# Performance work log

Measured on AMD Instinct MI355X. Metric: run time of the kernel, lower is better.

The kernel has to match this reference:

```python
import jax, jax.numpy as jnp
import numpy as np

N_NODES = 20000
N_EDGES = 50000
IN_DIM = 128
HID = 128
OUT_DIM = 64
N_PAIRS = 128
N_LAYERS = 2
N_HEADS = 4


def setup_inputs() -> dict:
    key = jax.random.key(0)
    ks = jax.random.split(key, 32)
    s = 0.05
    def p(k, shape):
        return jax.random.normal(k, shape, jnp.float32) * s
    inp = {}
    inp["node_features"] = jax.random.normal(ks[0], (N_NODES, IN_DIM), jnp.float32)
    inp["edge_index"] = jax.random.randint(ks[1], (2, N_EDGES), 0, N_NODES, jnp.int32)
    inp["edge_timestamps"] = jax.random.uniform(ks[2], (N_EDGES,), jnp.float32)
    inp["target_pairs"] = jax.random.randint(ks[3], (N_PAIRS, 2), 0, N_NODES, jnp.int32)
    inp["in_W"] = p(ks[4], (HID, IN_DIM)); inp["in_b"] = p(ks[5], (HID,))
    inp["te_W1"] = p(ks[6], (N_LAYERS, HID, 1)); inp["te_b1"] = p(ks[7], (N_LAYERS, HID))
    inp["te_W2"] = p(ks[8], (N_LAYERS, HID, HID)); inp["te_b2"] = p(ks[9], (N_LAYERS, HID))
    inp["attn_in_W"] = p(ks[10], (N_LAYERS, 3 * HID, HID)); inp["attn_in_b"] = p(ks[11], (N_LAYERS, 3 * HID))
    inp["attn_out_W"] = p(ks[12], (N_LAYERS, HID, HID)); inp["attn_out_b"] = p(ks[13], (N_LAYERS, HID))
    inp["ft_W"] = p(ks[14], (N_LAYERS, HID, HID)); inp["ft_b"] = p(ks[15], (N_LAYERS, HID))
    inp["op_W"] = p(ks[16], (N_LAYERS, HID, HID)); inp["op_b"] = p(ks[17], (N_LAYERS, HID))
    inp["out1_W"] = p(ks[18], (HID, HID)); inp["out1_b"] = p(ks[19], (HID,))
    inp["out2_W"] = p(ks[20], (OUT_DIM, HID)); inp["out2_b"] = p(ks[21], (OUT_DIM,))
    inp["lp1_W"] = p(ks[22], (HID, 2 * OUT_DIM)); inp["lp1_b"] = p(ks[23], (HID,))
    inp["lp2_W"] = p(ks[24], (HID // 2, HID)); inp["lp2_b"] = p(ks[25], (HID // 2,))
    inp["lp3_W"] = p(ks[26], (1, HID // 2)); inp["lp3_b"] = p(ks[27], (1,))
    return inp


def _forward(node_features, edge_index, edge_timestamps, target_pairs,
             in_W, in_b, te_W1, te_b1, te_W2, te_b2,
             attn_in_W, attn_in_b, attn_out_W, attn_out_b,
             ft_W, ft_b, op_W, op_b,
             out1_W, out1_b, out2_W, out2_b,
             lp1_W, lp1_b, lp2_W, lp2_b, lp3_W, lp3_b):
    N = node_features.shape[0]
    h = in_W.shape[0]
    H = N_HEADS
    d = h // H
    scale = 1.0 / np.sqrt(d).astype(np.float32)
    src, dst = edge_index[0], edge_index[1]
    # flattened target nodes; duplicates compute identical rows so dedup (torch.unique) is unneeded
    targets = target_pairs.reshape(-1)  # [U]
    U = targets.shape[0]
    E = src.shape[0]

    x = node_features @ in_W.T + in_b  # [N, h]
    for l in range(te_W1.shape[0]):
        tf = x @ ft_W[l].T + ft_b[l]                                           # [N, h]
        tfeat = jax.nn.relu(edge_timestamps[:, None] @ te_W1[l].T + te_b1[l])
        tfeat = tfeat @ te_W2[l].T + te_b2[l]                                  # [E, h]
        Wq, Wk, Wv = jnp.split(attn_in_W[l], 3, axis=0)
        bq, bk, bv = jnp.split(attn_in_b[l], 3)
        q = (tf[targets] @ Wq.T + bq).reshape(U, H, d)
        # keys/values are linear in (tf[nbr] + tfeat): split into node term A and edge term B
        Ak = (tf @ Wk.T).reshape(N, H, d)
        Bk = (tfeat @ Wk.T + bk).reshape(E, H, d)
        Av = (tf @ Wv.T).reshape(N, H, d)
        Bv = (tfeat @ Wv.T + bv).reshape(E, H, d)
        is_src = src[None, :] == targets[:, None]          # [U, E]
        mask = is_src | (dst[None, :] == targets[:, None])  # edge incident to target
        nbr = jnp.where(is_src, dst[None, :], src[None, :])  # other endpoint, [U, E]
        qAk = jnp.einsum('uhd,nhd->uhn', q, Ak) * scale      # [U, H, N]
        idx = jnp.broadcast_to(nbr[:, None, :], (U, H, E))
        s_node = jnp.take_along_axis(qAk, idx, axis=2)        # [U, H, E]
        s_edge = jnp.einsum('uhd,ehd->uhe', q, Bk) * scale
        scores = jnp.where(mask[:, None, :], s_node + s_edge, -1e30)
        p = jax.nn.softmax(scores, axis=-1)
        p = jnp.where(mask[:, None, :], p, 0.0)               # [U, H, E]
        out_edge = jnp.einsum('uhe,ehd->uhd', p, Bv)
        # sum_e p * Av[nbr] via per-target scatter of probs into node space
        w = jax.vmap(lambda pe, ne: jax.ops.segment_sum(pe, ne, num_segments=N))(
            p.transpose(0, 2, 1), nbr)                        # [U, N, H]
        out_node = jnp.einsum('unh,nhd->uhd', w, Av)
        attn = (out_node + out_edge).reshape(U, h) @ attn_out_W[l].T + attn_out_b[l]
        has_nbr = mask.any(axis=1)
        agg_in = jnp.where(has_nbr[:, None], attn, tf[targets])
        agg = agg_in @ op_W[l].T + op_b[l]
        x = x.at[targets].set(agg)
        x = jax.nn.relu(x)
    emb = jax.nn.relu(x @ out1_W.T + out1_b) @ out2_W.T + out2_b  # [N, out]
    pair = jnp.concatenate([emb[target_pairs[:, 0]], emb[target_pairs[:, 1]]], axis=1)
    z = jax.nn.relu(pair @ lp1_W.T + lp1_b)
    z = jax.nn.relu(z @ lp2_W.T + lp2_b)
    return jax.nn.sigmoid(z @ lp3_W.T + lp3_b)  # [B, 1]


def reference(node_features, edge_index, edge_timestamps, target_pairs,
              in_W, in_b, te_W1, te_b1, te_W2, te_b2,
              attn_in_W, attn_in_b, attn_out_W, attn_out_b,
              ft_W, ft_b, op_W, op_b,
              out1_W, out1_b, out2_W, out2_b,
              lp1_W, lp1_b, lp2_W, lp2_b, lp3_W, lp3_b):
    return _forward(node_features, edge_index, edge_timestamps, target_pairs,
                    in_W, in_b, te_W1, te_b1, te_W2, te_b2,
                    attn_in_W, attn_in_b, attn_out_W, attn_out_b,
                    ft_W, ft_b, op_W, op_b,
                    out1_W, out1_b, out2_W, out2_b,
                    lp1_W, lp1_b, lp2_W, lp2_b, lp3_W, lp3_b)
```

## Files before the change

### kernel.cpp

```cpp
#include <hip/hip_runtime.h>
#include <math.h>

#define N_NODES 20000
#define N_EDGES 50000
#define N_SLOTS 256
#define N_PAIRS 128
#define CAP 64
#define MSTRIDE 16384
#define NMAT 19

__device__ __forceinline__ float4 relu4(float4 v) {
    return make_float4(fmaxf(v.x, 0.f), fmaxf(v.y, 0.f), fmaxf(v.z, 0.f), fmaxf(v.w, 0.f));
}
__device__ __forceinline__ float4 add4(float4 a, float4 b) {
    return make_float4(a.x + b.x, a.y + b.y, a.z + b.z, a.w + b.w);
}
__device__ __forceinline__ void fma4(float4& acc, const float4 w, const float s) {
    acc.x = fmaf(w.x, s, acc.x); acc.y = fmaf(w.y, s, acc.y);
    acc.z = fmaf(w.z, s, acc.z); acc.w = fmaf(w.w, s, acc.w);
}
#define F4Z make_float4(0.f, 0.f, 0.f, 0.f)

__device__ __forceinline__ float4 mv_ks1(const float* __restrict__ WT,
                                         const float* __restrict__ xv128,
                                         int g, int jj) {
    const float4* W4 = (const float4*)WT;
    const float4* x4 = (const float4*)xv128;
    float4 acc = F4Z;
#pragma unroll 2
    for (int kk4 = 0; kk4 < 8; ++kk4) {
        int k4 = g * 8 + kk4;
        float4 xv = x4[k4];
        fma4(acc, W4[(k4 * 4 + 0) * 32 + jj], xv.x);
        fma4(acc, W4[(k4 * 4 + 1) * 32 + jj], xv.y);
        fma4(acc, W4[(k4 * 4 + 2) * 32 + jj], xv.z);
        fma4(acc, W4[(k4 * 4 + 3) * 32 + jj], xv.w);
    }
    return acc;
}
__device__ __forceinline__ float4 mv_ks1_64(const float* __restrict__ WT,
                                            const float* __restrict__ xv128,
                                            int g, int jj) {
    const float4* W4 = (const float4*)WT;
    const float4* x4 = (const float4*)xv128;
    int j16 = jj & 15;
    float4 acc = F4Z;
#pragma unroll 2
    for (int kk4 = 0; kk4 < 8; ++kk4) {
        int k4 = g * 8 + kk4;
        float4 xv = x4[k4];
        fma4(acc, W4[(k4 * 4 + 0) * 16 + j16], xv.x);
        fma4(acc, W4[(k4 * 4 + 1) * 16 + j16], xv.y);
        fma4(acc, W4[(k4 * 4 + 2) * 16 + j16], xv.z);
        fma4(acc, W4[(k4 * 4 + 3) * 16 + j16], xv.w);
    }
    return acc;
}
__device__ __forceinline__ float4 comb1(const float4* pb, int jj) {
    return add4(add4(pb[jj], pb[32 + jj]), add4(pb[64 + jj], pb[96 + jj]));
}

__device__ __forceinline__ float4 mv_ks1_g8(const float* __restrict__ WT,
                                            const float* __restrict__ xv128,
                                            int g, int jj) {
    const float4* W4 = (const float4*)WT;
    const float4* x4 = (const float4*)xv128;
    float4 acc = F4Z;
#pragma unroll
    for (int kk4 = 0; kk4 < 4; ++kk4) {
        int k4 = g * 4 + kk4;
        float4 xv = x4[k4];
        fma4(acc, W4[(k4 * 4 + 0) * 32 + jj], xv.x);
        fma4(acc, W4[(k4 * 4 + 1) * 32 + jj], xv.y);
        fma4(acc, W4[(k4 * 4 + 2) * 32 + jj], xv.z);
        fma4(acc, W4[(k4 * 4 + 3) * 32 + jj], xv.w);
    }
    return acc;
}
__device__ __forceinline__ void mv8_g8(const float* __restrict__ WT,
                                       const float* __restrict__ xs,
                                       int g, int jj, float4* acc) {
    const float4* W4 = (const float4*)WT;
    const float4* x4 = (const float4*)xs;
#pragma unroll
    for (int kk4 = 0; kk4 < 4; ++kk4) {
        int k4 = g * 4 + kk4;
        float4 w0 = W4[(k4 * 4 + 0) * 32 + jj];
        float4 w1 = W4[(k4 * 4 + 1) * 32 + jj];
        float4 w2 = W4[(k4 * 4 + 2) * 32 + jj];
        float4 w3 = W4[(k4 * 4 + 3) * 32 + jj];
#pragma unroll
        for (int e = 0; e < 8; ++e) {
            float4 xv = x4[e * 32 + k4];
            fma4(acc[e], w0, xv.x); fma4(acc[e], w1, xv.y);
            fma4(acc[e], w2, xv.z); fma4(acc[e], w3, xv.w);
        }
    }
}
__device__ __forceinline__ float4 comb1_g8(const float4* pb, int jj) {
    float4 s = pb[jj];
#pragma unroll
    for (int gp = 1; gp < 8; ++gp) s = add4(s, pb[gp * 32 + jj]);
    return s;
}
__device__ __forceinline__ float4 comb8_g8(const float4* pb, int it, int jj) {
    float4 s = pb[it * 32 + jj];
#pragma unroll
    for (int gp = 1; gp < 8; ++gp) s = add4(s, pb[(gp * 8 + it) * 32 + jj]);
    return s;
}


__global__ __launch_bounds__(256) void k_prep_tr(
    const int* __restrict__ ei, const int* __restrict__ tp,
    const float* __restrict__ inW, const float* __restrict__ ftW,
    const float* __restrict__ teW2, const float* __restrict__ aiW,
    const float* __restrict__ aoW, const float* __restrict__ opW,
    const float* __restrict__ o1W, const float* __restrict__ o2W,
    const float* __restrict__ l1W, const float* __restrict__ l2W,
    float* __restrict__ WT, int* __restrict__ cnt, int2* __restrict__ lst) {
    __shared__ float tile[32][129];
    __shared__ int lc;
    const int b = blockIdx.x;
    if (threadIdx.x == 0) lc = 0;
    if (b < 72) {
        int m, r0, rows;
        if (b < 68) { m = b >> 2; r0 = (b & 3) * 32; rows = 128; }
        else { int mm = b - 68; m = 17 + (mm >> 1); r0 = (mm & 1) * 32; rows = 64; }
        const float* src;
        if (m == 0) src = inW;
        else if (m <= 2) src = ftW + (m - 1) * MSTRIDE;
        else if (m <= 4) src = teW2 + (m - 3) * MSTRIDE;
        else if (m <= 10) src = aiW + (m - 5) * MSTRIDE;
        else if (m <= 12) src = aoW + (m - 11) * MSTRIDE;
        else if (m <= 14) src = opW + (m - 13) * MSTRIDE;
        else if (m == 15) src = o1W;
        else if (m == 16) src = l1W;
        else if (m == 17) src = o2W;
        else src = l2W;
        float* dst = WT + m * MSTRIDE;
        for (int idx = threadIdx.x; idx < 32 * 128; idx += 256) {
            int r = idx >> 7, c = idx & 127;
            tile[r][c] = src[(r0 + r) * 128 + c];
        }
        __syncthreads();
        for (int idx = threadIdx.x; idx < 128 * 32; idx += 256) {
            int k = idx >> 5, jr = idx & 31;
            dst[k * rows + r0 + jr] = tile[jr][k];
        }
    }
    __syncthreads();
    const int u = tp[b];
    const int4* src4 = (const int4*)ei;
    const int4* dst4 = (const int4*)(ei + N_EDGES);
    for (int e4 = threadIdx.x; e4 < N_EDGES / 4; e4 += 256) {
        int4 s = src4[e4];
        int4 d = dst4[e4];
        int ss[4] = {s.x, s.y, s.z, s.w};
        int dd[4] = {d.x, d.y, d.z, d.w};
#pragma unroll
        for (int t = 0; t < 4; ++t) {
            if (ss[t] == u || dd[t] == u) {
                int nbr = (ss[t] == u) ? dd[t] : ss[t];
                int pos = atomicAdd(&lc, 1);
                if (pos < CAP) lst[b * CAP + pos] = make_int2(e4 * 4 + t, nbr);
            }
        }
    }
    __syncthreads();
    if (threadIdx.x == 0) cnt[b] = lc;
}

__global__ __launch_bounds__(256) void k_edge(
    const float* __restrict__ nf, const float* __restrict__ x,
    const float* __restrict__ ts, const int* __restrict__ tp,
    const int* __restrict__ cnt, const int2* __restrict__ lst,
    const float* __restrict__ WT_in, const float* __restrict__ inb,
    const float* __restrict__ WT_ft, const float* __restrict__ ftb,
    const float* __restrict__ teW1, const float* __restrict__ teb1,
    const float* __restrict__ WT_te2, const float* __restrict__ teb2,
    const float* __restrict__ WT_q, const float* __restrict__ bq,
    const float* __restrict__ WT_k, const float* __restrict__ bk,
    const float* __restrict__ WT_v, const float* __restrict__ bv,
    float* __restrict__ x_out, float* __restrict__ tfu_g,
    float* __restrict__ scores, float* __restrict__ vbuf, int layer) {
    __shared__ __align__(16) float xu[128], x0u[128], tfv[128], qv[128];
    __shared__ __align__(16) float xs[8 * 128], t1s[8 * 128], x0s[8 * 128], zs[8 * 128];
    __shared__ __align__(16) float4 pb[8 * 8 * 32];
    __shared__ int nbr_s[8];
    __shared__ float ts_s[8];
    const int slot = blockIdx.x, tid = threadIdx.x, g = tid >> 5, jj = tid & 31;
    const float scale = 0.17677669529663687f;
    const int u = tp[slot];
    const int c = min(cnt[slot], CAP);

    if (tid < 128) xu[tid] = (layer == 0) ? nf[(size_t)u * 128 + tid]
                                          : x[(size_t)u * 128 + tid];
    __syncthreads();
    const float* xeff = xu;
    if (layer == 0) {
        pb[g * 32 + jj] = mv_ks1_g8(WT_in, xu, g, jj);
        __syncthreads();
        if (g == 0)
            *(float4*)(x0u + jj * 4) = add4(comb1_g8(pb, jj), *(const float4*)(inb + jj * 4));
        xeff = x0u;
        __syncthreads();
    }
    pb[g * 32 + jj] = mv_ks1_g8(WT_ft, xeff, g, jj);
    __syncthreads();
    if (g == 0) {
        float4 t = add4(comb1_g8(pb, jj), *(const float4*)(ftb + jj * 4));
        *(float4*)(tfv + jj * 4) = t;
        *(float4*)(tfu_g + (size_t)slot * 128 + jj * 4) = t;
    }
    __syncthreads();
    pb[g * 32 + jj] = mv_ks1_g8(WT_q, tfv, g, jj);
    __syncthreads();
    if (g == 0)
        *(float4*)(qv + jj * 4) = add4(comb1_g8(pb, jj), *(const float4*)(bq + jj * 4));
    __syncthreads();

    for (int base = 0; base < c; base += 8) {
        if (tid < 8) {
            int i = base + tid;
            int2 en = (i < c) ? lst[slot * CAP + i] : make_int2(0, 0);
            nbr_s[tid] = en.y;
            ts_s[tid] = (i < c) ? ts[en.x] : 0.f;
        }
        __syncthreads();
        {
            int e = tid >> 5, c0 = jj * 4;
            const float* srcp = (layer == 0) ? (nf + (size_t)nbr_s[e] * 128 + c0)
                                             : (x + (size_t)nbr_s[e] * 128 + c0);
            float4 v = *(const float4*)srcp;
            float* dstp = (layer == 0) ? xs : x0s;
            *(float4*)(dstp + e * 128 + c0) = v;
            float tse = ts_s[e];
            float4 w = *(const float4*)(teW1 + c0);
            float4 b = *(const float4*)(teb1 + c0);
            *(float4*)(t1s + e * 128 + c0) =
                make_float4(fmaxf(fmaf(tse, w.x, b.x), 0.f),
                            fmaxf(fmaf(tse, w.y, b.y), 0.f),
                            fmaxf(fmaf(tse, w.z, b.z), 0.f),
                            fmaxf(fmaf(tse, w.w, b.w), 0.f));
        }
        __syncthreads();
        if (layer == 0) {
            float4 acc[8] = {F4Z, F4Z, F4Z, F4Z, F4Z, F4Z, F4Z, F4Z};
            mv8_g8(WT_in, xs, g, jj, acc);
#pragma unroll
            for (int e = 0; e < 8; ++e) pb[(g * 8 + e) * 32 + jj] = acc[e];
            __syncthreads();
            {
                float4 x0v = add4(comb8_g8(pb, g, jj), *(const float4*)(inb + jj * 4));
                *(float4*)(x0s + g * 128 + jj * 4) = x0v;
                if (base + g < c)
                    *(float4*)(x_out + (size_t)nbr_s[g] * 128 + jj * 4) = relu4(x0v);
            }
            __syncthreads();
        }
        float4 za, zb;
        {
            float4 acc[8] = {F4Z, F4Z, F4Z, F4Z, F4Z, F4Z, F4Z, F4Z};
            mv8_g8(WT_ft, x0s, g, jj, acc);
#pragma unroll
            for (int e = 0; e < 8; ++e) pb[(g * 8 + e) * 32 + jj] = acc[e];
            __syncthreads();
            za = comb8_g8(pb, g, jj);
            __syncthreads();
            float4 acc2[8] = {F4Z, F4Z, F4Z, F4Z, F4Z, F4Z, F4Z, F4Z};
            mv8_g8(WT_te2, t1s, g, jj, acc2);
#pragma unroll
            for (int e = 0; e < 8; ++e) pb[(g * 8 + e) * 32 + jj] = acc2[e];
            __syncthreads();
            zb = comb8_g8(pb, g, jj);
            float4 z4 = add4(add4(za, zb),
                             add4(*(const float4*)(ftb + jj * 4),
                                  *(const float4*)(teb2 + jj * 4)));
            *(float4*)(zs + g * 128 + jj * 4) = z4;
            __syncthreads();
        }
        {
            float4 acc[8] = {F4Z, F4Z, F4Z, F4Z, F4Z, F4Z, F4Z, F4Z};
            mv8_g8(WT_k, zs, g, jj, acc);
#pragma unroll
            for (int e = 0; e < 8; ++e) pb[(g * 8 + e) * 32 + jj] = acc[e];
            __syncthreads();
            float4 kk = add4(comb8_g8(pb, g, jj), *(const float4*)(bk + jj * 4));
            __syncthreads();
            float4 acc2[8] = {F4Z, F4Z, F4Z, F4Z, F4Z, F4Z, F4Z, F4Z};
            mv8_g8(WT_v, zs, g, jj, acc2);
#pragma unroll
            for (int e = 0; e < 8; ++e) pb[(g * 8 + e) * 32 + jj] = acc2[e];
            __syncthreads();
            float4 vv = add4(comb8_g8(pb, g, jj), *(const float4*)(bv + jj * 4));
            float4 q4 = *(const float4*)(qv + jj * 4);
            float pr = q4.x * kk.x + q4.y * kk.y + q4.z * kk.z + q4.w * kk.w;
            pr += __shfl_xor(pr, 1);
            pr += __shfl_xor(pr, 2);
            pr += __shfl_xor(pr, 4);
            if (base + g < c) {
                int pos = slot * CAP + base + g;
                if ((jj & 7) == 0) scores[pos * 4 + (jj >> 3)] = pr * scale;
                *(float4*)(vbuf + (size_t)pos * 128 + jj * 4) = vv;
            }
            __syncthreads();
        }
    }
}

__global__ __launch_bounds__(128) void k_reduce(
    const int* __restrict__ cnt, const int* __restrict__ tp,
    const float* __restrict__ scores, const float* __restrict__ vbuf,
    const float* __restrict__ tfu_g,
    const float* __restrict__ WT_ao, const float* __restrict__ aob,
    const float* __restrict__ WT_op, const float* __restrict__ opb,
    float* __restrict__ x,
    const float* __restrict__ WT_o1, const float* __restrict__ o1b,
    const float* __restrict__ WT_o2, const float* __restrict__ o2b,
    float* __restrict__ emb, int mode) {
    __shared__ __align__(16) float outv[128], zv[128], xt[128], e1[128];
    __shared__ __align__(16) float4 pb[4 * 32];
    const int slot = blockIdx.x, tid = threadIdx.x, g = tid >> 5, jj = tid & 31;
    const int j = tid, h = j >> 5;
    const int u = tp[slot];
    const int c = min(cnt[slot], CAP);
    if (c > 0) {
        float m = -INFINITY;
        for (int i = 0; i < c; ++i) m = fmaxf(m, scores[(slot * CAP + i) * 4 + h]);
        float l = 0.f, o = 0.f;
        for (int i = 0; i < c; ++i) {
            float p = __expf(scores[(slot * CAP + i) * 4 + h] - m);
            l += p;
            o = fmaf(p, vbuf[(size_t)(slot * CAP + i) * 128 + j], o);
        }
        outv[j] = o / l;
    } else {
        outv[j] = 0.f;
    }
    __syncthreads();
    pb[g * 32 + jj] = mv_ks1(WT_ao, outv, g, jj);
    __syncthreads();
    if (g == 0) {
        float4 z4;
        if (c > 0) z4 = add4(comb1(pb, jj), *(const float4*)(aob + jj * 4));
        else z4 = *(const float4*)(tfu_g + (size_t)slot * 128 + jj * 4);
        *(float4*)(zv + jj * 4) = z4;
    }
    __syncthreads();
    pb[g * 32 + jj] = mv_ks1(WT_op, zv, g, jj);
    __syncthreads();
    if (mode == 0) {
        if (g == 0) {
            float4 a = relu4(add4(comb1(pb, jj), *(const float4*)(opb + jj * 4)));
            *(float4*)(x + (size_t)u * 128 + jj * 4) = a;
        }
        return;
    }
    if (g == 0)
        *(float4*)(xt + jj * 4) = relu4(add4(comb1(pb, jj), *(const float4*)(opb + jj * 4)));
    __syncthreads();
    pb[g * 32 + jj] = mv_ks1(WT_o1, xt, g, jj);
    __syncthreads();
    if (g == 0)
        *(float4*)(e1 + jj * 4) = relu4(add4(comb1(pb, jj), *(const float4*)(o1b + jj * 4)));
    __syncthreads();
    pb[g * 32 + jj] = mv_ks1_64(WT_o2, e1, g, jj);
    __syncthreads();
    if (g == 0 && jj < 16)
        *(float4*)(emb + (size_t)slot * 64 + jj * 4) =
            add4(comb1(pb, jj), *(const float4*)(o2b + jj * 4));
}

__global__ __launch_bounds__(128) void k_pair(
    const float* __restrict__ emb,
    const float* __restrict__ WT_l1, const float* __restrict__ l1b,
    const float* __restrict__ WT_l2, const float* __restrict__ l2b,
    const float* __restrict__ l3W, const float* __restrict__ l3b,
    float* __restrict__ out) {
    __shared__ __align__(16) float pv[128], z1[128], z2s[64];
    __shared__ __align__(16) float4 pb[4 * 32];
    const int p = blockIdx.x, tid = threadIdx.x, g = tid >> 5, jj = tid & 31;
    pv[tid] = (tid < 64) ? emb[(size_t)(2 * p) * 64 + tid]
                         : emb[(size_t)(2 * p + 1) * 64 + (tid - 64)];
    __syncthreads();
    pb[g * 32 + jj] = mv_ks1(WT_l1, pv, g, jj);
    __syncthreads();
    if (g == 0)
        *(float4*)(z1 + jj * 4) = relu4(add4(comb1(pb, jj), *(const float4*)(l1b + jj * 4)));
    __syncthreads();
    pb[g * 32 + jj] = mv_ks1_64(WT_l2, z1, g, jj);
    __syncthreads();
    if (g == 0 && jj < 16)
        *(float4*)(z2s + jj * 4) = relu4(add4(comb1(pb, jj), *(const float4*)(l2b + jj * 4)));
    __syncthreads();
    if (tid < 64) {
        float v = z2s[tid] * l3W[tid];
        v += __shfl_xor(v, 1);
        v += __shfl_xor(v, 2);
        v += __shfl_xor(v, 4);
        v += __shfl_xor(v, 8);
        v += __shfl_xor(v, 16);
        v += __shfl_xor(v, 32);
        if (tid == 0) out[p] = 1.f / (1.f + __expf(-(v + l3b[0])));
    }
}

extern "C" void kernel_launch(void* const* d_in, const int* in_sizes, int n_in,
                              void* d_out, int out_size, void* d_ws, size_t ws_size,
                              hipStream_t stream) {
    const float* nf  = (const float*)d_in[0];
    const int*   ei  = (const int*)d_in[1];
    const float* ts  = (const float*)d_in[2];
    const int*   tp  = (const int*)d_in[3];
    const float* inW = (const float*)d_in[4];
    const float* inb = (const float*)d_in[5];
    const float* teW1 = (const float*)d_in[6];
    const float* teb1 = (const float*)d_in[7];
    const float* teW2 = (const float*)d_in[8];
    const float* teb2 = (const float*)d_in[9];
    const float* aiW = (const float*)d_in[10];
    const float* aib = (const float*)d_in[11];
    const float* aoW = (const float*)d_in[12];
    const float* aob = (const float*)d_in[13];
    const float* ftW = (const float*)d_in[14];
    const float* ftb = (const float*)d_in[15];
    const float* opW = (const float*)d_in[16];
    const float* opb = (const float*)d_in[17];
    const float* o1W = (const float*)d_in[18];
    const float* o1b = (const float*)d_in[19];
    const float* o2W = (const float*)d_in[20];
    const float* o2b = (const float*)d_in[21];
    const float* l1W = (const float*)d_in[22];
    const float* l1b = (const float*)d_in[23];
    const float* l2W = (const float*)d_in[24];
    const float* l2b = (const float*)d_in[25];
    const float* l3W = (const float*)d_in[26];
    const float* l3b = (const float*)d_in[27];
    float* out = (float*)d_out;

    char* ws = (char*)d_ws;
    size_t off = 0;
    float* x    = (float*)(ws + off); off += (size_t)N_NODES * 128 * 4;
    int*   cnt  = (int*)  (ws + off); off += N_SLOTS * 4;
    int2*  lst  = (int2*) (ws + off); off += (size_t)N_SLOTS * CAP * 8;
    float* tfu  = (float*)(ws + off); off += N_SLOTS * 128 * 4;
    float* emb  = (float*)(ws + off); off += N_SLOTS * 64 * 4;
    float* scb  = (float*)(ws + off); off += (size_t)N_SLOTS * CAP * 4 * 4;
    float* vbuf = (float*)(ws + off); off += (size_t)N_SLOTS * CAP * 128 * 4;
    float* WT   = (float*)(ws + off); off += (size_t)NMAT * MSTRIDE * 4;

    k_prep_tr<<<N_SLOTS, 256, 0, stream>>>(ei, tp, inW, ftW, teW2, aiW, aoW, opW,
                                           o1W, o2W, l1W, l2W, WT, cnt, lst);

    for (int l = 0; l < 2; ++l) {
        const float* WT_ft = WT + (1 + l) * MSTRIDE;
        const float* WT_te2 = WT + (3 + l) * MSTRIDE;
        const float* WT_q = WT + (5 + 3 * l) * MSTRIDE;
        const float* WT_k = WT + (6 + 3 * l) * MSTRIDE;
        const float* WT_v = WT + (7 + 3 * l) * MSTRIDE;
        const float* WT_ao = WT + (11 + l) * MSTRIDE;
        const float* WT_op = WT + (13 + l) * MSTRIDE;
        const float* bq = aib + l * 384;
        k_edge<<<N_SLOTS, 256, 0, stream>>>(
            nf, x, ts, tp, cnt, lst,
            WT, inb, WT_ft, ftb + l * 128, teW1 + l * 128, teb1 + l * 128,
            WT_te2, teb2 + l * 128, WT_q, bq, WT_k, bq + 128, WT_v, bq + 256,
            x, tfu, scb, vbuf, l);
        k_reduce<<<N_SLOTS, 128, 0, stream>>>(
            cnt, tp, scb, vbuf, tfu, WT_ao, aob + l * 128,
            WT_op, opb + l * 128, x,
            WT + 15 * MSTRIDE, o1b, WT + 17 * MSTRIDE, o2b, emb, l);
    }
    k_pair<<<N_PAIRS, 128, 0, stream>>>(emb, WT + 16 * MSTRIDE, l1b,
                                        WT + 18 * MSTRIDE, l2b, l3W, l3b, out);
}
```

Before: 205.1 us.

## Fuse edge and reduce kernels per layer, keep scores and values in shared memory

The per-layer edge kernel and the softmax/reduce kernel are merged into one k_layer kernel. Attention scores and value vectors now stay in shared memory instead of round-tripping through global buffers, and the tf vector is kept on-chip. To avoid a race where a neighbour write in one block would clobber a target row written by another block in the same kernel, the prep kernel marks neighbours that are themselves targets with a flag bit, and those writes are skipped. This removes a launch and global traffic per layer, but raises shared memory per block (about 32KB for the value buffer), which may lower occupancy.

```diff
diff --git a/kernel.cpp b/kernel.cpp
--- a/kernel.cpp
+++ b/kernel.cpp
@@ -8,6 +8,7 @@
 #define CAP 64
 #define MSTRIDE 16384
 #define NMAT 19
+#define TFLAG (1 << 30)
 
 __device__ __forceinline__ float4 relu4(float4 v) {
     return make_float4(fmaxf(v.x, 0.f), fmaxf(v.y, 0.f), fmaxf(v.z, 0.f), fmaxf(v.w, 0.f));
@@ -20,6 +21,74 @@
     acc.z = fmaf(w.z, s, acc.z); acc.w = fmaf(w.w, s, acc.w);
 }
 #define F4Z make_float4(0.f, 0.f, 0.f, 0.f)
+
+__device__ __forceinline__ float4 mv_ks1_g8(const float* __restrict__ WT,
+                                            const float* __restrict__ xv128,
+                                            int g, int jj) {
+    const float4* W4 = (const float4*)WT;
+    const float4* x4 = (const float4*)xv128;
+    float4 acc = F4Z;
+#pragma unroll
+    for (int kk4 = 0; kk4 < 4; ++kk4) {
+        int k4 = g * 4 + kk4;
+        float4 xv = x4[k4];
+        fma4(acc, W4[(k4 * 4 + 0) * 32 + jj], xv.x);
+        fma4(acc, W4[(k4 * 4 + 1) * 32 + jj], xv.y);
+        fma4(acc, W4[(k4 * 4 + 2) * 32 + jj], xv.z);
+        fma4(acc, W4[(k4 * 4 + 3) * 32 + jj], xv.w);
+    }
+    return acc;
+}
+__device__ __forceinline__ float4 mv_ks1_g8_64(const float* __restrict__ WT,
+                                               const float* __restrict__ xv128,
+                                               int g, int jj) {
+    const float4* W4 = (const float4*)WT;
+    const float4* x4 = (const float4*)xv128;
+    int j16 = jj & 15;
+    float4 acc = F4Z;
+#pragma unroll
+    for (int kk4 = 0; kk4 < 4; ++kk4) {
+        int k4 = g * 4 + kk4;
+        float4 xv = x4[k4];
+        fma4(acc, W4[(k4 * 4 + 0) * 16 + j16], xv.x);
+        fma4(acc, W4[(k4 * 4 + 1) * 16 + j16], xv.y);
+        fma4(acc, W4[(k4 * 4 + 2) * 16 + j16], xv.z);
+        fma4(acc, W4[(k4 * 4 + 3) * 16 + j16], xv.w);
+    }
+    return acc;
+}
+__device__ __forceinline__ void mv8_g8(const float* __restrict__ WT,
+                                       const float* __restrict__ xs,
+                                       int g, int jj, float4* acc) {
+    const float4* W4 = (const float4*)WT;
+    const float4* x4 = (const float4*)xs;
+#pragma unroll
+    for (int kk4 = 0; kk4 < 4; ++kk4) {
+        int k4 = g * 4 + kk4;
+        float4 w0 = W4[(k4 * 4 + 0) * 32 + jj];
+        float4 w1 = W4[(k4 * 4 + 1) * 32 + jj];
+        float4 w2 = W4[(k4 * 4 + 2) * 32 + jj];
+        float4 w3 = W4[(k4 * 4 + 3) * 32 + jj];
+#pragma unroll
+        for (int e = 0; e < 8; ++e) {
+            float4 xv = x4[e * 32 + k4];
+            fma4(acc[e], w0, xv.x); fma4(acc[e], w1, xv.y);
+            fma4(acc[e], w2, xv.z); fma4(acc[e], w3, xv.w);
+        }
+    }
+}
+__device__ __forceinline__ float4 comb1_g8(const float4* pb, int jj) {
+    float4 s = pb[jj];
+#pragma unroll
+    for (int gp = 1; gp < 8; ++gp) s = add4(s, pb[gp * 32 + jj]);
+    return s;
+}
+__device__ __forceinline__ float4 comb8_g8(const float4* pb, int it, int jj) {
+    float4 s = pb[it * 32 + jj];
+#pragma unroll
+    for (int gp = 1; gp < 8; ++gp) s = add4(s, pb[(gp * 8 + it) * 32 + jj]);
+    return s;
+}
 
 __device__ __forceinline__ float4 mv_ks1(const float* __restrict__ WT,
                                          const float* __restrict__ xv128,
@@ -60,56 +129,6 @@
     return add4(add4(pb[jj], pb[32 + jj]), add4(pb[64 + jj], pb[96 + jj]));
 }
 
-__device__ __forceinline__ float4 mv_ks1_g8(const float* __restrict__ WT,
-                                            const float* __restrict__ xv128,
-                                            int g, int jj) {
-    const float4* W4 = (const float4*)WT;
-    const float4* x4 = (const float4*)xv128;
-    float4 acc = F4Z;
-#pragma unroll
-    for (int kk4 = 0; kk4 < 4; ++kk4) {
-        int k4 = g * 4 + kk4;
-        float4 xv = x4[k4];
-        fma4(acc, W4[(k4 * 4 + 0) * 32 + jj], xv.x);
-        fma4(acc, W4[(k4 * 4 + 1) * 32 + jj], xv.y);
-        fma4(acc, W4[(k4 * 4 + 2) * 32 + jj], xv.z);
-        fma4(acc, W4[(k4 * 4 + 3) * 32 + jj], xv.w);
-    }
-    return acc;
-}
-__device__ __forceinline__ void mv8_g8(const float* __restrict__ WT,
-                                       const float* __restrict__ xs,
-                                       int g, int jj, float4* acc) {
-    const float4* W4 = (const float4*)WT;
-    const float4* x4 = (const float4*)xs;
-#pragma unroll
-    for (int kk4 = 0; kk4 < 4; ++kk4) {
-        int k4 = g * 4 + kk4;
-        float4 w0 = W4[(k4 * 4 + 0) * 32 + jj];
-        float4 w1 = W4[(k4 * 4 + 1) * 32 + jj];
-        float4 w2 = W4[(k4 * 4 + 2) * 32 + jj];
-        float4 w3 = W4[(k4 * 4 + 3) * 32 + jj];
-#pragma unroll
-        for (int e = 0; e < 8; ++e) {
-            float4 xv = x4[e * 32 + k4];
-            fma4(acc[e], w0, xv.x); fma4(acc[e], w1, xv.y);
-            fma4(acc[e], w2, xv.z); fma4(acc[e], w3, xv.w);
-        }
-    }
-}
-__device__ __forceinline__ float4 comb1_g8(const float4* pb, int jj) {
-    float4 s = pb[jj];
-#pragma unroll
-    for (int gp = 1; gp < 8; ++gp) s = add4(s, pb[gp * 32 + jj]);
-    return s;
-}
-__device__ __forceinline__ float4 comb8_g8(const float4* pb, int it, int jj) {
-    float4 s = pb[it * 32 + jj];
-#pragma unroll
-    for (int gp = 1; gp < 8; ++gp) s = add4(s, pb[(gp * 8 + it) * 32 + jj]);
-    return s;
-}
-
 
 __global__ __launch_bounds__(256) void k_prep_tr(
     const int* __restrict__ ei, const int* __restrict__ tp,
@@ -120,6 +139,7 @@
     const float* __restrict__ l1W, const float* __restrict__ l2W,
     float* __restrict__ WT, int* __restrict__ cnt, int2* __restrict__ lst) {
     __shared__ float tile[32][129];
+    __shared__ int tps[N_SLOTS];
     __shared__ int lc;
     const int b = blockIdx.x;
     if (threadIdx.x == 0) lc = 0;
@@ -149,8 +169,9 @@
             dst[k * rows + r0 + jr] = tile[jr][k];
         }
     }
-    __syncthreads();
-    const int u = tp[b];
+    for (int i = threadIdx.x; i < N_SLOTS; i += 256) tps[i] = tp[i];
+    __syncthreads();
+    const int u = tps[b];
     const int4* src4 = (const int4*)ei;
     const int4* dst4 = (const int4*)(ei + N_EDGES);
     for (int e4 = threadIdx.x; e4 < N_EDGES / 4; e4 += 256) {
@@ -169,9 +190,16 @@
     }
     __syncthreads();
     if (threadIdx.x == 0) cnt[b] = lc;
-}
-
-__global__ __launch_bounds__(256) void k_edge(
+    int c = min(lc, CAP);
+    if (threadIdx.x < c) {
+        int2 en = lst[b * CAP + threadIdx.x];
+        bool ist = false;
+        for (int t = 0; t < N_SLOTS; ++t) ist |= (tps[t] == en.y);
+        if (ist) { en.y |= TFLAG; lst[b * CAP + threadIdx.x] = en; }
+    }
+}
+
+__global__ __launch_bounds__(256) void k_layer(
     const float* __restrict__ nf, const float* __restrict__ x,
     const float* __restrict__ ts, const int* __restrict__ tp,
     const int* __restrict__ cnt, const int2* __restrict__ lst,
@@ -182,12 +210,17 @@
     const float* __restrict__ WT_q, const float* __restrict__ bq,
     const float* __restrict__ WT_k, const float* __restrict__ bk,
     const float* __restrict__ WT_v, const float* __restrict__ bv,
-    float* __restrict__ x_out, float* __restrict__ tfu_g,
-    float* __restrict__ scores, float* __restrict__ vbuf, int layer) {
-    __shared__ __align__(16) float xu[128], x0u[128], tfv[128], qv[128];
+    const float* __restrict__ WT_ao, const float* __restrict__ aob,
+    const float* __restrict__ WT_op, const float* __restrict__ opb,
+    const float* __restrict__ WT_o1, const float* __restrict__ o1b,
+    const float* __restrict__ WT_o2, const float* __restrict__ o2b,
+    float* __restrict__ x_out, float* __restrict__ emb, int layer) {
+    __shared__ __align__(16) float xu[128], x0u[128], tfv[128], qv[128], sv[128];
     __shared__ __align__(16) float xs[8 * 128], t1s[8 * 128], x0s[8 * 128], zs[8 * 128];
     __shared__ __align__(16) float4 pb[8 * 8 * 32];
-    __shared__ int nbr_s[8];
+    __shared__ __align__(16) float vbl[CAP * 128];
+    __shared__ float scl[CAP * 4];
+    __shared__ int nbr_s[8], tf_s[8];
     __shared__ float ts_s[8];
     const int slot = blockIdx.x, tid = threadIdx.x, g = tid >> 5, jj = tid & 31;
     const float scale = 0.17677669529663687f;
@@ -208,11 +241,8 @@
     }
     pb[g * 32 + jj] = mv_ks1_g8(WT_ft, xeff, g, jj);
     __syncthreads();
-    if (g == 0) {
-        float4 t = add4(comb1_g8(pb, jj), *(const float4*)(ftb + jj * 4));
-        *(float4*)(tfv + jj * 4) = t;
-        *(float4*)(tfu_g + (size_t)slot * 128 + jj * 4) = t;
-    }
+    if (g == 0)
+        *(float4*)(tfv + jj * 4) = add4(comb1_g8(pb, jj), *(const float4*)(ftb + jj * 4));
     __syncthreads();
     pb[g * 32 + jj] = mv_ks1_g8(WT_q, tfv, g, jj);
     __syncthreads();
@@ -224,7 +254,8 @@
         if (tid < 8) {
             int i = base + tid;
             int2 en = (i < c) ? lst[slot * CAP + i] : make_int2(0, 0);
-            nbr_s[tid] = en.y;
+            nbr_s[tid] = en.y & ~TFLAG;
+            tf_s[tid] = (en.y & TFLAG) ? 1 : 0;
             ts_s[tid] = (i < c) ? ts[en.x] : 0.f;
         }
         __syncthreads();
@@ -254,26 +285,25 @@
             {
                 float4 x0v = add4(comb8_g8(pb, g, jj), *(const float4*)(inb + jj * 4));
                 *(float4*)(x0s + g * 128 + jj * 4) = x0v;
-                if (base + g < c)
+                if (base + g < c && !tf_s[g])
                     *(float4*)(x_out + (size_t)nbr_s[g] * 128 + jj * 4) = relu4(x0v);
             }
             __syncthreads();
         }
-        float4 za, zb;
         {
             float4 acc[8] = {F4Z, F4Z, F4Z, F4Z, F4Z, F4Z, F4Z, F4Z};
             mv8_g8(WT_ft, x0s, g, jj, acc);
 #pragma unroll
             for (int e = 0; e < 8; ++e) pb[(g * 8 + e) * 32 + jj] = acc[e];
             __syncthreads();
-            za = comb8_g8(pb, g, jj);
+            float4 za = comb8_g8(pb, g, jj);
             __syncthreads();
             float4 acc2[8] = {F4Z, F4Z, F4Z, F4Z, F4Z, F4Z, F4Z, F4Z};
             mv8_g8(WT_te2, t1s, g, jj, acc2);
 #pragma unroll
             for (int e = 0; e < 8; ++e) pb[(g * 8 + e) * 32 + jj] = acc2[e];
             __syncthreads();
-            zb = comb8_g8(pb, g, jj);
+            float4 zb = comb8_g8(pb, g, jj);
             float4 z4 = add4(add4(za, zb),
                              add4(*(const float4*)(ftb + jj * 4),
                                   *(const float4*)(teb2 + jj * 4)));
@@ -300,76 +330,63 @@
             pr += __shfl_xor(pr, 2);
             pr += __shfl_xor(pr, 4);
             if (base + g < c) {
-                int pos = slot * CAP + base + g;
-                if ((jj & 7) == 0) scores[pos * 4 + (jj >> 3)] = pr * scale;
-                *(float4*)(vbuf + (size_t)pos * 128 + jj * 4) = vv;
+                if ((jj & 7) == 0) scl[(base + g) * 4 + (jj >> 3)] = pr * scale;
+                *(float4*)(vbl + (base + g) * 128 + jj * 4) = vv;
             }
             __syncthreads();
         }
     }
-}
-
-__global__ __launch_bounds__(128) void k_reduce(
-    const int* __restrict__ cnt, const int* __restrict__ tp,
-    const float* __restrict__ scores, const float* __restrict__ vbuf,
-    const float* __restrict__ tfu_g,
-    const float* __restrict__ WT_ao, const float* __restrict__ aob,
-    const float* __restrict__ WT_op, const float* __restrict__ opb,
-    float* __restrict__ x,
-    const float* __restrict__ WT_o1, const float* __restrict__ o1b,
-    const float* __restrict__ WT_o2, const float* __restrict__ o2b,
-    float* __restrict__ emb, int mode) {
-    __shared__ __align__(16) float outv[128], zv[128], xt[128], e1[128];
-    __shared__ __align__(16) float4 pb[4 * 32];
-    const int slot = blockIdx.x, tid = threadIdx.x, g = tid >> 5, jj = tid & 31;
-    const int j = tid, h = j >> 5;
-    const int u = tp[slot];
-    const int c = min(cnt[slot], CAP);
-    if (c > 0) {
-        float m = -INFINITY;
-        for (int i = 0; i < c; ++i) m = fmaxf(m, scores[(slot * CAP + i) * 4 + h]);
-        float l = 0.f, o = 0.f;
-        for (int i = 0; i < c; ++i) {
-            float p = __expf(scores[(slot * CAP + i) * 4 + h] - m);
-            l += p;
-            o = fmaf(p, vbuf[(size_t)(slot * CAP + i) * 128 + j], o);
-        }
-        outv[j] = o / l;
-    } else {
-        outv[j] = 0.f;
-    }
-    __syncthreads();
-    pb[g * 32 + jj] = mv_ks1(WT_ao, outv, g, jj);
+
+    if (tid < 128) {
+        int h = tid >> 5;
+        if (c > 0) {
+            float m = -INFINITY;
+            for (int i = 0; i < c; ++i) m = fmaxf(m, scl[i * 4 + h]);
+            float l = 0.f, o = 0.f;
+            for (int i = 0; i < c; ++i) {
+                float p = __expf(scl[i * 4 + h] - m);
+                l += p;
+                o = fmaf(p, vbl[i * 128 + tid], o);
+            }
+            sv[tid] = o / l;
+        } else {
+            sv[tid] = 0.f;
+        }
+    }
+    __syncthreads();
+    pb[g * 32 + jj] = mv_ks1_g8(WT_ao, sv, g, jj);
     __syncthreads();
     if (g == 0) {
         float4 z4;
-        if (c > 0) z4 = add4(comb1(pb, jj), *(const float4*)(aob + jj * 4));
-        else z4 = *(const float4*)(tfu_g + (size_t)slot * 128 + jj * 4);
-        *(float4*)(zv + jj * 4) = z4;
-    }
-    __syncthreads();
-    pb[g * 32 + jj] = mv_ks1(WT_op, zv, g, jj);
-    __syncthreads();
-    if (mode == 0) {
+        if (c > 0) z4 = add4(comb1_g8(pb, jj), *(const float4*)(aob + jj * 4));
+        else z4 = *(const float4*)(tfv + jj * 4);
+        *(float4*)(xu + jj * 4) = z4;
+    }
+    __syncthreads();
+    pb[g * 32 + jj] = mv_ks1_g8(WT_op, xu, g, jj);
+    __syncthreads();
+    if (layer == 0) {
         if (g == 0) {
-            float4 a = relu4(add4(comb1(pb, jj), *(const float4*)(opb + jj * 4)));
-            *(float4*)(x + (size_t)u * 128 + jj * 4) = a;
+            float4 a = relu4(add4(comb1_g8(pb, jj), *(const float4*)(opb + jj * 4)));
+            *(float4*)(x_out + (size_t)u * 128 + jj * 4) = a;
         }
         return;
     }
     if (g == 0)
-        *(float4*)(xt + jj * 4) = relu4(add4(comb1(pb, jj), *(const float4*)(opb + jj * 4)));
-    __syncthreads();
-    pb[g * 32 + jj] = mv_ks1(WT_o1, xt, g, jj);
+        *(float4*)(x0u + jj * 4) =
+            relu4(add4(comb1_g8(pb, jj), *(const float4*)(opb + jj * 4)));
+    __syncthreads();
+    pb[g * 32 + jj] = mv_ks1_g8(WT_o1, x0u, g, jj);
     __syncthreads();
     if (g == 0)
-        *(float4*)(e1 + jj * 4) = relu4(add4(comb1(pb, jj), *(const float4*)(o1b + jj * 4)));
-    __syncthreads();
-    pb[g * 32 + jj] = mv_ks1_64(WT_o2, e1, g, jj);
+        *(float4*)(tfv + jj * 4) =
+            relu4(add4(comb1_g8(pb, jj), *(const float4*)(o1b + jj * 4)));
+    __syncthreads();
+    pb[g * 32 + jj] = mv_ks1_g8_64(WT_o2, tfv, g, jj);
     __syncthreads();
     if (g == 0 && jj < 16)
         *(float4*)(emb + (size_t)slot * 64 + jj * 4) =
-            add4(comb1(pb, jj), *(const float4*)(o2b + jj * 4));
+            add4(comb1_g8(pb, jj), *(const float4*)(o2b + jj * 4));
 }
 
 __global__ __launch_bounds__(128) void k_pair(
@@ -444,10 +461,7 @@
     float* x    = (float*)(ws + off); off += (size_t)N_NODES * 128 * 4;
     int*   cnt  = (int*)  (ws + off); off += N_SLOTS * 4;
     int2*  lst  = (int2*) (ws + off); off += (size_t)N_SLOTS * CAP * 8;
-    float* tfu  = (float*)(ws + off); off += N_SLOTS * 128 * 4;
     float* emb  = (float*)(ws + off); off += N_SLOTS * 64 * 4;
-    float* scb  = (float*)(ws + off); off += (size_t)N_SLOTS * CAP * 4 * 4;
-    float* vbuf = (float*)(ws + off); off += (size_t)N_SLOTS * CAP * 128 * 4;
     float* WT   = (float*)(ws + off); off += (size_t)NMAT * MSTRIDE * 4;
 
     k_prep_tr<<<N_SLOTS, 256, 0, stream>>>(ei, tp, inW, ftW, teW2, aiW, aoW, opW,
@@ -462,15 +476,13 @@
         const float* WT_ao = WT + (11 + l) * MSTRIDE;
         const float* WT_op = WT + (13 + l) * MSTRIDE;
         const float* bq = aib + l * 384;
-        k_edge<<<N_SLOTS, 256, 0, stream>>>(
+        k_layer<<<N_SLOTS, 256, 0, stream>>>(
             nf, x, ts, tp, cnt, lst,
             WT, inb, WT_ft, ftb + l * 128, teW1 + l * 128, teb1 + l * 128,
             WT_te2, teb2 + l * 128, WT_q, bq, WT_k, bq + 128, WT_v, bq + 256,
-            x, tfu, scb, vbuf, l);
-        k_reduce<<<N_SLOTS, 128, 0, stream>>>(
-            cnt, tp, scb, vbuf, tfu, WT_ao, aob + l * 128,
-            WT_op, opb + l * 128, x,
-            WT + 15 * MSTRIDE, o1b, WT + 17 * MSTRIDE, o2b, emb, l);
+            WT_ao, aob + l * 128, WT_op, opb + l * 128,
+            WT + 15 * MSTRIDE, o1b, WT + 17 * MSTRIDE, o2b,
+            x, emb, l);
     }
     k_pair<<<N_PAIRS, 128, 0, stream>>>(emb, WT + 16 * MSTRIDE, l1b,
                                         WT + 18 * MSTRIDE, l2b, l3W, l3b, out);
```

Result: faster. 200.9 us (-2.1%).
